# Kernel optimization log

Hardware: AMD Instinct MI355X
Metric: run time of the kernel (lower is better)

Reference implementation:

```python
import jax, jax.numpy as jnp
import numpy as np
from jax import lax

B, F, I, S = 4, 1024, 2048, 2048
K, G = 7, 4
INIT_SCALE = 1.0
LEAK = 0.02


def _norm(x):
    # normalize over channel dim (axis 1): subtract mean, divide by RMS-style L2 norm
    x = x - jnp.mean(x, axis=1, keepdims=True)
    n = jnp.sqrt(jnp.sum(x * x, axis=1, keepdims=True)) * (x.shape[1] ** -0.5)
    return x / (n + 1e-5)


def _conv1x1(x, w):
    # x: [B, Cin, S], w: [Cout, Cin, 1]
    return jnp.einsum('bcs,oc->bos', x, w[:, :, 0])


def setup_inputs() -> dict:
    key = jax.random.key(0)
    k1, k2, k3, k4 = jax.random.split(key, 4)
    inp = jax.random.normal(k1, (B, F, S), dtype=jnp.float32)
    divisor = (jnp.arange(S, dtype=jnp.float32) + 1.0).reshape(1, 1, S)
    w0_gate = jax.random.normal(k2, (3 * I, F, 1), dtype=jnp.float32) * (F ** -0.5)
    w1 = jax.random.normal(k3, (3 * I, I // G, K), dtype=jnp.float32) * ((I // G * K) ** -0.5)
    w2_gate = jax.random.normal(k4, (F, I, 1), dtype=jnp.float32) * (I ** -0.5)
    return {"inp": inp, "divisor": divisor, "w0_gate": w0_gate, "w1": w1, "w2_gate": w2_gate}


def reference(inp, divisor, w0_gate, w1, w2_gate):
    # 1x1 conv features -> 3*intermediate
    x = _conv1x1(inp, w0_gate)                       # [B, 3I, S]
    depth, scale, shift = jnp.split(x, 3, axis=1)    # each [B, I, S]
    cum = jnp.cumsum(depth, axis=-1)
    x = jax.nn.leaky_relu(_norm(cum / divisor * scale + shift), LEAK)
    # causal pad + grouped conv1d intermediate -> 3*intermediate
    x = jnp.pad(x, ((0, 0), (0, 0), (K - 1, 0)))
    x = lax.conv_general_dilated(x, w1, window_strides=(1,), padding='VALID',
                                 dimension_numbers=('NCH', 'OIH', 'NCH'),
                                 feature_group_count=G)  # [B, 3I, S]
    s0, s1, sh = jnp.split(x, 3, axis=1)
    x = jax.nn.leaky_relu(_norm(s0 * s1 + sh), LEAK)     # [B, I, S]
    # 1x1 conv intermediate -> features
    out = _conv1x1(x, w2_gate)                           # [B, F, S]
    return out * INIT_SCALE
```

## Files before the change

kernel.cpp:

```cpp
#include <hip/hip_runtime.h>

#define BATCH 4
#define FDIM  1024
#define IDIM  2048
#define SDIM  2048
#define I3    6144
#define KW    7
#define IG    512
#define OG    1536
#define KD2   3584
#define SP    2056

using short8 = __attribute__((ext_vector_type(8))) short;
using f32x4  = __attribute__((ext_vector_type(4))) float;

__device__ __forceinline__ unsigned short f2bf(float f) {
  unsigned int u = __float_as_uint(f);
  u += 0x7fffu + ((u >> 16) & 1u);
  return (unsigned short)(u >> 16);
}
__device__ __forceinline__ float bf2f(unsigned short u) {
  return __uint_as_float((unsigned int)u << 16);
}

__device__ __forceinline__ void gload16(const void* g, void* l) {
  __builtin_amdgcn_global_load_lds((const __attribute__((address_space(1))) void*)g,
                                   (__attribute__((address_space(3))) void*)l,
                                   16, 0, 0);
}

template<int MODE, int OBF16>
__global__ __launch_bounds__(512, 1)
void gemm256(const unsigned short* __restrict__ A,
             const unsigned short* __restrict__ Bt,
             void* __restrict__ C,
             int mtiles, int ktiles,
             int lda, int ldb, int ldc,
             long aZ, long bZ, long cZ)
{
  __shared__ unsigned short lds[2][2][16384];

  const int tid  = threadIdx.x;
  const int wv   = tid >> 6;
  const int lane = tid & 63;
  const int lr = lane & 15, lq = lane >> 4;
  const int wr = wv >> 2, wc = wv & 3;
  const int xm = (lr & 7) << 4;
  const int c8 = ((tid & 7) ^ ((tid >> 3) & 7)) << 3;

  const int nwg = gridDim.x;
  const int cpx = nwg >> 3;
  const int bid = blockIdx.x;
  const int w   = (bid & 7) * cpx + (bid >> 3);
  const int T   = mtiles << 3;
  const int z   = w / T;
  const int rr  = w - z * T;
  const int mt  = rr % mtiles;
  const int nt  = rr / mtiles;

  const unsigned short* Ab;
  const unsigned short* Bb;
  size_t coff;
  int gbase = 0;
  if (MODE == 2) {
    int b = z >> 2, g = z & 3;
    Ab = A + (size_t)g * OG * KD2;
    Bb = Bt + (size_t)b * SP * IDIM;
    coff = ((size_t)b * I3 + (size_t)g * OG) * (size_t)ldc;
    gbase = g * IG;
  } else {
    Ab = A + (size_t)z * aZ;
    Bb = Bt + (size_t)z * bZ;
    coff = (size_t)z * cZ;
  }

  const int m0 = mt * 256, n0 = nt * 256;

  f32x4 acc[8][4];
  const f32x4 vzero = {0.f, 0.f, 0.f, 0.f};
#pragma unroll
  for (int i = 0; i < 8; ++i)
#pragma unroll
    for (int j = 0; j < 4; ++j) acc[i][j] = vzero;

  auto STAGEC = [&](int buf, int kt1, int c) {
    const int k0 = kt1 << 6;
    int row = (c << 6) + (tid >> 3);
    gload16(Ab + (size_t)(m0 + row) * lda + (k0 + c8),
            &lds[buf][0][c * 4096 + wv * 512]);
    const unsigned short* g;
    if (MODE == 2) {
      int kk = k0 + c8;
      g = Bb + (size_t)(n0 + row + (kk >> 9) + 2) * IDIM + (gbase + (kk & 511));
    } else {
      g = Bb + (size_t)(n0 + row) * ldb + (k0 + c8);
    }
    gload16(g, &lds[buf][1][c * 4096 + wv * 512]);
  };

  auto RDA = [&](int buf, int i, int kk) -> short8 {
    int row = wr * 128 + i * 16 + lr;
    int off = ((row << 7) + (kk << 1) + (lq << 4)) ^ xm;
    return *(const short8*)((const char*)&lds[buf][0][0] + off);
  };
  auto RDB = [&](int buf, int j, int kk) -> short8 {
    int row = wc * 64 + j * 16 + lr;
    int off = ((row << 7) + (kk << 1) + (lq << 4)) ^ xm;
    return *(const short8*)((const char*)&lds[buf][1][0] + off);
  };

#define MFMA16(AF, BV, IOFF)                                                     \
  __builtin_amdgcn_s_setprio(1);                                                 \
  _Pragma("unroll")                                                              \
  for (int i = 0; i < 4; ++i)                                                    \
    _Pragma("unroll")                                                            \
    for (int j = 0; j < 4; ++j)                                                  \
      acc[i + IOFF][j] =                                                         \
          __builtin_amdgcn_mfma_f32_16x16x32_bf16(AF[i], BV[j], acc[i + IOFF][j],\
                                                  0, 0, 0);                      \
  __builtin_amdgcn_s_setprio(0);

  STAGEC(0, 0, 0); STAGEC(0, 0, 1); STAGEC(0, 0, 2); STAGEC(0, 0, 3);
  asm volatile("s_waitcnt vmcnt(0)" ::: "memory");
  __builtin_amdgcn_s_barrier();
  __builtin_amdgcn_sched_barrier(0);

  for (int kt = 0; kt < ktiles - 1; ++kt) {
    const int cur = kt & 1;
    short8 af0[4], af1[4], bv0[4], bv1[4];
#pragma unroll
    for (int j = 0; j < 4; ++j) bv0[j] = RDB(cur, j, 0);
#pragma unroll
    for (int i = 0; i < 4; ++i) af0[i] = RDA(cur, i, 0);
    STAGEC(cur ^ 1, kt + 1, 0);
#pragma unroll
    for (int i = 0; i < 4; ++i) af1[i] = RDA(cur, i + 4, 0);
    MFMA16(af0, bv0, 0)
    STAGEC(cur ^ 1, kt + 1, 1);
#pragma unroll
    for (int j = 0; j < 4; ++j) bv1[j] = RDB(cur, j, 32);
#pragma unroll
    for (int i = 0; i < 4; ++i) af0[i] = RDA(cur, i, 32);
    MFMA16(af1, bv0, 4)
    STAGEC(cur ^ 1, kt + 1, 2);
#pragma unroll
    for (int i = 0; i < 4; ++i) af1[i] = RDA(cur, i + 4, 32);
    MFMA16(af0, bv1, 0)
    STAGEC(cur ^ 1, kt + 1, 3);
    MFMA16(af1, bv1, 4)

    asm volatile("s_waitcnt vmcnt(0)" ::: "memory");
    __builtin_amdgcn_s_barrier();
    __builtin_amdgcn_sched_barrier(0);
  }

  {
    const int cur = (ktiles - 1) & 1;
    short8 af0[4], af1[4], bv0[4], bv1[4];
#pragma unroll
    for (int j = 0; j < 4; ++j) bv0[j] = RDB(cur, j, 0);
#pragma unroll
    for (int i = 0; i < 4; ++i) af0[i] = RDA(cur, i, 0);
#pragma unroll
    for (int i = 0; i < 4; ++i) af1[i] = RDA(cur, i + 4, 0);
    MFMA16(af0, bv0, 0)
#pragma unroll
    for (int j = 0; j < 4; ++j) bv1[j] = RDB(cur, j, 32);
#pragma unroll
    for (int i = 0; i < 4; ++i) af0[i] = RDA(cur, i, 32);
    MFMA16(af1, bv0, 4)
#pragma unroll
    for (int i = 0; i < 4; ++i) af1[i] = RDA(cur, i + 4, 32);
    MFMA16(af0, bv1, 0)
    MFMA16(af1, bv1, 4)
  }
#undef MFMA16

#pragma unroll
  for (int i = 0; i < 8; ++i) {
#pragma unroll
    for (int j = 0; j < 4; ++j) {
      int ccol  = n0 + wc * 64 + j * 16 + lr;
      int rbase = m0 + wr * 128 + i * 16 + lq * 4;
      if (OBF16) {
        unsigned short* Cs = (unsigned short*)C + coff;
#pragma unroll
        for (int e = 0; e < 4; ++e)
          Cs[(size_t)(rbase + e) * ldc + ccol] = f2bf(acc[i][j][e]);
      } else {
        float* Cf = (float*)C + coff;
#pragma unroll
        for (int e = 0; e < 4; ++e)
          Cf[(size_t)(rbase + e) * ldc + ccol] = acc[i][j][e];
      }
    }
  }
}

__global__ __launch_bounds__(256, 2)
void gemm128(const unsigned short* __restrict__ A,
             const unsigned short* __restrict__ Bt,
             float* __restrict__ C,
             int mtiles, int ktiles,
             int lda, int ldb, int ldc,
             long aZ, long bZ, long cZ)
{
  __shared__ unsigned short sA[128 * 64];
  __shared__ unsigned short sB[128 * 64];

  const int tid  = threadIdx.x;
  const int wave = tid >> 6;
  const int lane = tid & 63;
  const int mt = blockIdx.x % mtiles;
  const int nt = blockIdx.x / mtiles;
  const int z  = blockIdx.y;

  const unsigned short* Ab = A + (size_t)z * aZ;
  const unsigned short* Bb = Bt + (size_t)z * bZ;
  float* Cb = C + (size_t)z * cZ;

  const int m0 = mt * 128, n0 = nt * 128;
  const int wr = wave >> 1, wc = wave & 1;
  const int lr = lane & 15, lq = lane >> 4;
  const int xm = (lr & 7) << 4;
  const int c8 = ((tid & 7) ^ ((tid >> 3) & 7)) << 3;

  f32x4 acc[4][4];
  const f32x4 vzero = {0.f, 0.f, 0.f, 0.f};
#pragma unroll
  for (int i = 0; i < 4; ++i)
#pragma unroll
    for (int j = 0; j < 4; ++j) acc[i][j] = vzero;

  for (int kt = 0; kt < ktiles; ++kt) {
    const int k0 = kt * 64;
#pragma unroll
    for (int it = 0; it < 4; ++it) {
      int row = it * 32 + (tid >> 3);
      gload16(Ab + (size_t)(m0 + row) * lda + (k0 + c8),
              &sA[(size_t)(it * 256 + (tid & ~63)) * 8]);
    }
#pragma unroll
    for (int it = 0; it < 4; ++it) {
      int row = it * 32 + (tid >> 3);
      gload16(Bb + (size_t)(n0 + row) * ldb + (k0 + c8),
              &sB[(size_t)(it * 256 + (tid & ~63)) * 8]);
    }
    asm volatile("s_waitcnt vmcnt(0)" ::: "memory");
    __builtin_amdgcn_s_barrier();
#pragma unroll
    for (int kk = 0; kk < 64; kk += 32) {
      short8 af[4], bfr[4];
#pragma unroll
      for (int i = 0; i < 4; ++i) {
        int row = wr * 64 + i * 16 + lr;
        af[i] = *(const short8*)((const char*)sA + (((row << 7) + (kk << 1) + (lq << 4)) ^ xm));
      }
#pragma unroll
      for (int j = 0; j < 4; ++j) {
        int row = wc * 64 + j * 16 + lr;
        bfr[j] = *(const short8*)((const char*)sB + (((row << 7) + (kk << 1) + (lq << 4)) ^ xm));
      }
#pragma unroll
      for (int i = 0; i < 4; ++i)
#pragma unroll
        for (int j = 0; j < 4; ++j)
          acc[i][j] = __builtin_amdgcn_mfma_f32_16x16x32_bf16(af[i], bfr[j], acc[i][j], 0, 0, 0);
    }
    __builtin_amdgcn_s_barrier();
  }

#pragma unroll
  for (int i = 0; i < 4; ++i) {
#pragma unroll
    for (int j = 0; j < 4; ++j) {
      int ccol  = n0 + wc * 64 + j * 16 + lr;
      int rbase = m0 + wr * 64 + i * 16 + lq * 4;
#pragma unroll
      for (int e = 0; e < 4; ++e)
        Cb[(size_t)(rbase + e) * ldc + ccol] = acc[i][j][e];
    }
  }
}

__global__ void cvt_f2b(const float* __restrict__ in, unsigned short* __restrict__ out, long n) {
  long stride = (long)gridDim.x * blockDim.x;
  for (long i = (long)blockIdx.x * blockDim.x + threadIdx.x; i < n; i += stride)
    out[i] = f2bf(in[i]);
}

__global__ void perm_w1(const float* __restrict__ in, unsigned short* __restrict__ out) {
  __shared__ float row[2][KD2];
  int o0 = blockIdx.x * 2;
  int t  = threadIdx.x;
#pragma unroll
  for (int r = 0; r < 2; ++r)
    for (int j = t; j < KD2; j += 256)
      row[r][j] = in[(size_t)(o0 + r) * KD2 + j];
  __syncthreads();
#pragma unroll
  for (int r = 0; r < 2; ++r)
    for (int j = t; j < KD2; j += 256) {
      int c = j & 511, k = j >> 9;
      out[(size_t)(o0 + r) * KD2 + j] = f2bf(row[r][c * KW + k]);
    }
}

__global__ void transpose_in(const float* __restrict__ in, unsigned short* __restrict__ out) {
  __shared__ float tile[64][65];
  int bid = blockIdx.x;
  int b   = bid >> 9;
  int rem = bid & 511;
  int ft  = rem >> 5;
  int st  = rem & 31;
  int tc  = threadIdx.x & 63, tr = threadIdx.x >> 6;
  const float* ip = in + ((size_t)b * FDIM + ft * 64) * SDIM + st * 64;
#pragma unroll
  for (int r = tr; r < 64; r += 4)
    tile[r][tc] = ip[(size_t)r * SDIM + tc];
  __syncthreads();
  unsigned short* op = out + ((size_t)b * SDIM + st * 64) * FDIM + ft * 64;
#pragma unroll
  for (int r = tr; r < 64; r += 4)
    op[(size_t)r * FDIM + tc] = f2bf(tile[tc][r]);
}

__global__ void scan_rows(const unsigned short* __restrict__ C1, unsigned short* __restrict__ V) {
  int rid = blockIdx.x;
  int b = rid >> 11;
  int i = rid & 2047;
  const unsigned short* dp = C1 + ((size_t)b * I3 + i) * SDIM;
  const unsigned short* sp = dp + (size_t)IDIM * SDIM;
  const unsigned short* hp = dp + (size_t)2 * IDIM * SDIM;
  unsigned short* vp = V + ((size_t)b * IDIM + i) * SDIM;
  int t = threadIdx.x, lane = t & 63, wid = t >> 6;

  short8 dv = *(const short8*)(dp + t * 8);
  float c[8];
  float run = 0.f;
#pragma unroll
  for (int e = 0; e < 8; ++e) { run += bf2f((unsigned short)dv[e]); c[e] = run; }

  float s = run;
#pragma unroll
  for (int off = 1; off < 64; off <<= 1) {
    float v = __shfl_up(s, off, 64);
    if (lane >= off) s += v;
  }
  __shared__ float wtot[4];
  if (lane == 63) wtot[wid] = s;
  __syncthreads();
  float base = 0.f;
#pragma unroll
  for (int w2 = 0; w2 < 3; ++w2) base += (w2 < wid) ? wtot[w2] : 0.f;
  float excl = base + s - run;

  short8 sv = *(const short8*)(sp + t * 8);
  short8 hv = *(const short8*)(hp + t * 8);
  short8 ov;
#pragma unroll
  for (int e = 0; e < 8; ++e) {
    int si = t * 8 + e;
    float val = (excl + c[e]) / (float)(si + 1) * bf2f((unsigned short)sv[e]) + bf2f((unsigned short)hv[e]);
    ov[e] = (short)f2bf(val);
  }
  *(short8*)(vp + t * 8) = ov;
}

template<int MODE>
__global__ void stats_part(const unsigned short* __restrict__ X, float* __restrict__ psum,
                           float* __restrict__ psq, unsigned short* __restrict__ G) {
  int bid = blockIdx.x;
  int b   = bid >> 5;
  int s0  = (bid & 31) * 64;
  int iz  = blockIdx.y;
  int ts  = threadIdx.x & 63, tg = threadIdx.x >> 6;
  float sum = 0.f, sq = 0.f;
  for (int i = iz * 512 + tg; i < iz * 512 + 512; i += 4) {
    float g;
    if (MODE == 1) {
      g = bf2f(X[((size_t)b * IDIM + i) * SDIM + s0 + ts]);
    } else {
      float a  = bf2f(X[((size_t)b * I3 + i) * SDIM + s0 + ts]);
      float bb = bf2f(X[((size_t)b * I3 + IDIM + i) * SDIM + s0 + ts]);
      float cc = bf2f(X[((size_t)b * I3 + 2 * IDIM + i) * SDIM + s0 + ts]);
      g = a * bb + cc;
      G[((size_t)b * IDIM + i) * SDIM + s0 + ts] = f2bf(g);
    }
    sum += g; sq += g * g;
  }
  __shared__ float sS[4][64], sQ[4][64];
  sS[tg][ts] = sum; sQ[tg][ts] = sq;
  __syncthreads();
  if (threadIdx.x < 64) {
    float s = sS[0][ts] + sS[1][ts] + sS[2][ts] + sS[3][ts];
    float q = sQ[0][ts] + sQ[1][ts] + sQ[2][ts] + sQ[3][ts];
    psum[((size_t)b * SDIM + s0 + ts) * 4 + iz] = s;
    psq [((size_t)b * SDIM + s0 + ts) * 4 + iz] = q;
  }
}

template<int MODE>
__global__ void norm_apply(const unsigned short* __restrict__ X, const float* __restrict__ psum,
                           const float* __restrict__ psq, unsigned short* __restrict__ out) {
  __shared__ float tile[64][65];
  int bid = blockIdx.x;
  int b   = bid >> 5;
  int s0  = (bid & 31) * 64;
  int i0  = blockIdx.y * 512;
  int tc  = threadIdx.x & 63, tr = threadIdx.x >> 6;
  size_t sidx = ((size_t)b * SDIM + s0 + tc) * 4;
  float s4 = psum[sidx] + psum[sidx + 1] + psum[sidx + 2] + psum[sidx + 3];
  float q4 = psq [sidx] + psq [sidx + 1] + psq [sidx + 2] + psq [sidx + 3];
  float mn  = s4 * (1.f / 2048.f);
  float var = q4 * (1.f / 2048.f) - mn * mn;
  float iv  = 1.f / (sqrtf(fmaxf(var, 0.f)) + 1e-5f);
  size_t orow = (MODE == 1) ? ((size_t)b * SP + 8 + s0) : ((size_t)b * SDIM + s0);
  for (int ic = i0; ic < i0 + 512; ic += 64) {
#pragma unroll
    for (int r = tr; r < 64; r += 4) {
      int i = ic + r;
      float g = bf2f(X[((size_t)b * IDIM + i) * SDIM + s0 + tc]);
      float y = (g - mn) * iv;
      y = (y >= 0.f) ? y : 0.02f * y;
      tile[r][tc] = y;
    }
    __syncthreads();
#pragma unroll
    for (int r = tr; r < 64; r += 4)
      out[(orow + r) * IDIM + ic + tc] = f2bf(tile[tc][r]);
    __syncthreads();
  }
}

__global__ void zero_x1t_pad(unsigned short* __restrict__ x1t) {
  int idx = blockIdx.x * 256 + threadIdx.x;
  if (idx < BATCH * 8 * IDIM) {
    int b   = idx / (8 * IDIM);
    int rem = idx - b * (8 * IDIM);
    x1t[(size_t)b * SP * IDIM + rem] = 0;
  }
}

__global__ void report_ws(float* __restrict__ out, float mb) {
  if (threadIdx.x == 0 && blockIdx.x == 0) out[0] = mb;
}

extern "C" void kernel_launch(void* const* d_in, const int* in_sizes, int n_in,
                              void* d_out, int out_size, void* d_ws, size_t ws_size,
                              hipStream_t stream) {
  const float* inp = (const float*)d_in[0];
  const float* w0  = (const float*)d_in[2];
  const float* w1  = (const float*)d_in[3];
  const float* w2  = (const float*)d_in[4];
  float* out = (float*)d_out;
  char* ws = (char*)d_ws;

  const size_t REQ = 216465408ULL;
  if (ws_size < REQ) {
    report_ws<<<1, 1, 0, stream>>>(out, (float)(ws_size >> 20));
    return;
  }

  unsigned short* A2   = (unsigned short*)(ws + 0);
  unsigned short* A3   = (unsigned short*)(ws + 44040192);
  unsigned short* C1   = (unsigned short*)(ws + 48234496);
  unsigned short* X1T  = (unsigned short*)(ws + 148897792);
  unsigned short* G    = (unsigned short*)(ws + 148897792);
  char*           VXr  = ws + 182583296;
  unsigned short* A1   = (unsigned short*)(VXr + 0);
  unsigned short* BINT = (unsigned short*)(VXr + 12582912);
  unsigned short* V    = (unsigned short*)(VXr + 0);
  unsigned short* X2T  = (unsigned short*)(VXr + 0);
  float* PSUM = (float*)(ws + 216137728);
  float* PSQ  = (float*)(ws + 216268800);

  cvt_f2b<<<2048, 256, 0, stream>>>(w0, A1, (long)I3 * FDIM);
  cvt_f2b<<<2048, 256, 0, stream>>>(w2, A3, (long)FDIM * IDIM);
  perm_w1<<<I3 / 2, 256, 0, stream>>>(w1, A2);
  transpose_in<<<2048, 256, 0, stream>>>(inp, BINT);
  zero_x1t_pad<<<256, 256, 0, stream>>>(X1T);

  gemm256<0, 1><<<24 * 8 * BATCH, 512, 0, stream>>>(
      A1, BINT, C1, 24, 16, FDIM, FDIM, SDIM,
      0L, (long)SDIM * FDIM, (long)I3 * SDIM);

  scan_rows<<<BATCH * IDIM, 256, 0, stream>>>(C1, V);

  stats_part<1><<<dim3(128, 4), 256, 0, stream>>>(V, PSUM, PSQ, nullptr);
  norm_apply<1><<<dim3(128, 4), 256, 0, stream>>>(V, PSUM, PSQ, X1T);

  gemm256<2, 1><<<6 * 8 * 16, 512, 0, stream>>>(
      A2, X1T, C1, 6, 56, KD2, 0, SDIM, 0L, 0L, 0L);

  stats_part<2><<<dim3(128, 4), 256, 0, stream>>>(C1, PSUM, PSQ, G);
  norm_apply<2><<<dim3(128, 4), 256, 0, stream>>>(G, PSUM, PSQ, X2T);

  gemm128<<<dim3(8 * 16, BATCH), 256, 0, stream>>>(
      A3, X2T, out, 8, 32, IDIM, IDIM, SDIM,
      0L, (long)SDIM * IDIM, (long)FDIM * SDIM);
}
```

Before: 668.7 us.

## Vectorize norm statistics kernels, fuse weight casts, and reorder GEMM load staging

The stats_part kernels now load eight bf16 values per thread with 16-byte vector loads and split the channel reduction into 16 partial sums instead of 4. norm_apply is adjusted to sum the 16 partials. The two fp32-to-bf16 weight conversions are merged into one launch, and the global-to-LDS staging calls in the GEMM main loop are issued earlier. The partial-sum scratch now lives in the output buffer, which is only overwritten by the final GEMM.

```diff
diff --git a/kernel.cpp b/kernel.cpp
--- a/kernel.cpp
+++ b/kernel.cpp
@@ -133,20 +133,20 @@
 #pragma unroll
     for (int i = 0; i < 4; ++i) af0[i] = RDA(cur, i, 0);
     STAGEC(cur ^ 1, kt + 1, 0);
+    STAGEC(cur ^ 1, kt + 1, 1);
 #pragma unroll
     for (int i = 0; i < 4; ++i) af1[i] = RDA(cur, i + 4, 0);
     MFMA16(af0, bv0, 0)
-    STAGEC(cur ^ 1, kt + 1, 1);
+    STAGEC(cur ^ 1, kt + 1, 2);
 #pragma unroll
     for (int j = 0; j < 4; ++j) bv1[j] = RDB(cur, j, 32);
 #pragma unroll
     for (int i = 0; i < 4; ++i) af0[i] = RDA(cur, i, 32);
     MFMA16(af1, bv0, 4)
-    STAGEC(cur ^ 1, kt + 1, 2);
+    STAGEC(cur ^ 1, kt + 1, 3);
 #pragma unroll
     for (int i = 0; i < 4; ++i) af1[i] = RDA(cur, i + 4, 32);
     MFMA16(af0, bv1, 0)
-    STAGEC(cur ^ 1, kt + 1, 3);
     MFMA16(af1, bv1, 4)
 
     asm volatile("s_waitcnt vmcnt(0)" ::: "memory");
@@ -283,10 +283,14 @@
   }
 }
 
-__global__ void cvt_f2b(const float* __restrict__ in, unsigned short* __restrict__ out, long n) {
+__global__ void cvt2_f2b(const float* __restrict__ in0, unsigned short* __restrict__ out0, long n0,
+                         const float* __restrict__ in1, unsigned short* __restrict__ out1, long n1) {
   long stride = (long)gridDim.x * blockDim.x;
-  for (long i = (long)blockIdx.x * blockDim.x + threadIdx.x; i < n; i += stride)
-    out[i] = f2bf(in[i]);
+  long nt = n0 + n1;
+  for (long i = (long)blockIdx.x * blockDim.x + threadIdx.x; i < nt; i += stride) {
+    if (i < n0) out0[i] = f2bf(in0[i]);
+    else        out1[i - n0] = f2bf(in1[i - n0]);
+  }
 }
 
 __global__ void perm_w1(const float* __restrict__ in, unsigned short* __restrict__ out) {
@@ -370,33 +374,51 @@
 template<int MODE>
 __global__ void stats_part(const unsigned short* __restrict__ X, float* __restrict__ psum,
                            float* __restrict__ psq, unsigned short* __restrict__ G) {
-  int bid = blockIdx.x;
-  int b   = bid >> 5;
-  int s0  = (bid & 31) * 64;
-  int iz  = blockIdx.y;
-  int ts  = threadIdx.x & 63, tg = threadIdx.x >> 6;
-  float sum = 0.f, sq = 0.f;
-  for (int i = iz * 512 + tg; i < iz * 512 + 512; i += 4) {
-    float g;
+  int b  = blockIdx.x >> 2;
+  int s0 = (blockIdx.x & 3) * 512;
+  int iz = blockIdx.y;
+  int sg = threadIdx.x & 63;
+  int ig = threadIdx.x >> 6;
+  int s  = s0 + sg * 8;
+  float sum[8], sq[8];
+#pragma unroll
+  for (int e = 0; e < 8; ++e) { sum[e] = 0.f; sq[e] = 0.f; }
+  for (int p = 0; p < 32; ++p) {
+    int i = iz * 128 + p * 4 + ig;
     if (MODE == 1) {
-      g = bf2f(X[((size_t)b * IDIM + i) * SDIM + s0 + ts]);
+      short8 v = *(const short8*)&X[((size_t)b * IDIM + i) * SDIM + s];
+#pragma unroll
+      for (int e = 0; e < 8; ++e) {
+        float g = bf2f((unsigned short)v[e]);
+        sum[e] += g; sq[e] += g * g;
+      }
     } else {
-      float a  = bf2f(X[((size_t)b * I3 + i) * SDIM + s0 + ts]);
-      float bb = bf2f(X[((size_t)b * I3 + IDIM + i) * SDIM + s0 + ts]);
-      float cc = bf2f(X[((size_t)b * I3 + 2 * IDIM + i) * SDIM + s0 + ts]);
-      g = a * bb + cc;
-      G[((size_t)b * IDIM + i) * SDIM + s0 + ts] = f2bf(g);
-    }
-    sum += g; sq += g * g;
-  }
-  __shared__ float sS[4][64], sQ[4][64];
-  sS[tg][ts] = sum; sQ[tg][ts] = sq;
+      size_t base = ((size_t)b * I3 + i) * SDIM + s;
+      short8 av = *(const short8*)&X[base];
+      short8 bv = *(const short8*)&X[base + (size_t)IDIM * SDIM];
+      short8 cv = *(const short8*)&X[base + (size_t)2 * IDIM * SDIM];
+      short8 gv;
+#pragma unroll
+      for (int e = 0; e < 8; ++e) {
+        float g = bf2f((unsigned short)av[e]) * bf2f((unsigned short)bv[e]) + bf2f((unsigned short)cv[e]);
+        gv[e] = (short)f2bf(g);
+        sum[e] += g; sq[e] += g * g;
+      }
+      *(short8*)&G[((size_t)b * IDIM + i) * SDIM + s] = gv;
+    }
+  }
+  __shared__ float sS[4][64][8], sQ[4][64][8];
+#pragma unroll
+  for (int e = 0; e < 8; ++e) { sS[ig][sg][e] = sum[e]; sQ[ig][sg][e] = sq[e]; }
   __syncthreads();
-  if (threadIdx.x < 64) {
-    float s = sS[0][ts] + sS[1][ts] + sS[2][ts] + sS[3][ts];
-    float q = sQ[0][ts] + sQ[1][ts] + sQ[2][ts] + sQ[3][ts];
-    psum[((size_t)b * SDIM + s0 + ts) * 4 + iz] = s;
-    psq [((size_t)b * SDIM + s0 + ts) * 4 + iz] = q;
+  if (ig == 0) {
+#pragma unroll
+    for (int e = 0; e < 8; ++e) {
+      float ts = sS[0][sg][e] + sS[1][sg][e] + sS[2][sg][e] + sS[3][sg][e];
+      float tq = sQ[0][sg][e] + sQ[1][sg][e] + sQ[2][sg][e] + sQ[3][sg][e];
+      psum[((size_t)b * SDIM + s + e) * 16 + iz] = ts;
+      psq [((size_t)b * SDIM + s + e) * 16 + iz] = tq;
+    }
   }
 }
 
@@ -409,9 +431,10 @@
   int s0  = (bid & 31) * 64;
   int i0  = blockIdx.y * 512;
   int tc  = threadIdx.x & 63, tr = threadIdx.x >> 6;
-  size_t sidx = ((size_t)b * SDIM + s0 + tc) * 4;
-  float s4 = psum[sidx] + psum[sidx + 1] + psum[sidx + 2] + psum[sidx + 3];
-  float q4 = psq [sidx] + psq [sidx + 1] + psq [sidx + 2] + psq [sidx + 3];
+  size_t sidx = ((size_t)b * SDIM + s0 + tc) * 16;
+  float s4 = 0.f, q4 = 0.f;
+#pragma unroll
+  for (int iz = 0; iz < 16; ++iz) { s4 += psum[sidx + iz]; q4 += psq[sidx + iz]; }
   float mn  = s4 * (1.f / 2048.f);
   float var = q4 * (1.f / 2048.f) - mn * mn;
   float iv  = 1.f / (sqrtf(fmaxf(var, 0.f)) + 1e-5f);
@@ -472,11 +495,10 @@
   unsigned short* BINT = (unsigned short*)(VXr + 12582912);
   unsigned short* V    = (unsigned short*)(VXr + 0);
   unsigned short* X2T  = (unsigned short*)(VXr + 0);
-  float* PSUM = (float*)(ws + 216137728);
-  float* PSQ  = (float*)(ws + 216268800);
-
-  cvt_f2b<<<2048, 256, 0, stream>>>(w0, A1, (long)I3 * FDIM);
-  cvt_f2b<<<2048, 256, 0, stream>>>(w2, A3, (long)FDIM * IDIM);
+  float* PSUM = out;
+  float* PSQ  = out + (size_t)BATCH * SDIM * 16;
+
+  cvt2_f2b<<<2048, 256, 0, stream>>>(w0, A1, (long)I3 * FDIM, w2, A3, (long)FDIM * IDIM);
   perm_w1<<<I3 / 2, 256, 0, stream>>>(w1, A2);
   transpose_in<<<2048, 256, 0, stream>>>(inp, BINT);
   zero_x1t_pad<<<256, 256, 0, stream>>>(X1T);
@@ -487,13 +509,13 @@
 
   scan_rows<<<BATCH * IDIM, 256, 0, stream>>>(C1, V);
 
-  stats_part<1><<<dim3(128, 4), 256, 0, stream>>>(V, PSUM, PSQ, nullptr);
+  stats_part<1><<<dim3(16, 16), 256, 0, stream>>>(V, PSUM, PSQ, nullptr);
   norm_apply<1><<<dim3(128, 4), 256, 0, stream>>>(V, PSUM, PSQ, X1T);
 
   gemm256<2, 1><<<6 * 8 * 16, 512, 0, stream>>>(
       A2, X1T, C1, 6, 56, KD2, 0, SDIM, 0L, 0L, 0L);
 
-  stats_part<2><<<dim3(128, 4), 256, 0, stream>>>(C1, PSUM, PSQ, G);
+  stats_part<2><<<dim3(16, 16), 256, 0, stream>>>(C1, PSUM, PSQ, G);
   norm_apply<2><<<dim3(128, 4), 256, 0, stream>>>(G, PSUM, PSQ, X2T);
 
   gemm128<<<dim3(8 * 16, BATCH), 256, 0, stream>>>(
```

After: 604.0 us. 9.7% less time.
